# Kernel optimization log

Measured on AMD Instinct MI355X. Metric: run time of the kernel, lower is better.

## Reference

```python
import jax, jax.numpy as jnp
import numpy as np

T, B, I, H = 512, 256, 256, 512  # seq_len, batch, input_size, hidden_size


def setup_inputs() -> dict:
    key = jax.random.key(0)
    ks = jax.random.split(key, 7)
    sc = 1.0 / np.sqrt(H)  # PyTorch nn.RNN init scale ~ U(-1/sqrt(H), 1/sqrt(H)); use scaled normal
    return {
        "x": jax.random.normal(ks[0], (T, B, I), dtype=jnp.float32),
        "w_ih": jax.random.normal(ks[1], (H, I), dtype=jnp.float32) * sc,
        "w_hh": jax.random.normal(ks[2], (H, H), dtype=jnp.float32) * sc,
        "b_ih": jax.random.normal(ks[3], (H,), dtype=jnp.float32) * sc,
        "b_hh": jax.random.normal(ks[4], (H,), dtype=jnp.float32) * sc,
        "w_fc": jax.random.normal(ks[5], (I, H), dtype=jnp.float32) * sc,
        "b_fc": jax.random.normal(ks[6], (I,), dtype=jnp.float32) * sc,
    }


def reference(x, w_ih, w_hh, b_ih, b_hh, w_fc, b_fc):
    # Single-layer tanh RNN (h0 = 0): h_t = tanh(x_t W_ih^T + b_ih + h_{t-1} W_hh^T + b_hh)
    # Hoist the input projection out of the recurrence (one big GEMM).
    xp = jnp.einsum('tbi,hi->tbh', x, w_ih) + b_ih + b_hh  # [T,B,H]
    h0 = jnp.zeros((x.shape[1], w_hh.shape[0]), dtype=x.dtype)

    def step(h, xt):
        h_new = jnp.tanh(xt + h @ w_hh.T)
        return h_new, h_new

    _, hs = jax.lax.scan(step, h0, xp)  # hs: [T,B,H]
    # Output head: Linear(hidden_size -> input_size)
    return jnp.einsum('tbh,oh->tbo', hs, w_fc) + b_fc  # [T,B,I]
```

## Files before the change

### kernel.cpp

```cpp
#include <hip/hip_runtime.h>
#include <hip/hip_bf16.h>

#define T_ 512
#define B_ 256
#define I_ 256
#define H_ 512

#define NG 16
#define NS 4

#define RING_WPG (H_ * 8)
#define RING_BYTES (2ull * NG * RING_WPG * 8)

typedef _Float16 f16x8 __attribute__((ext_vector_type(8)));
typedef float f32x4 __attribute__((ext_vector_type(4)));

__device__ __forceinline__ float tanh_fast(float v) {
  float e = __expf(2.0f * v);
  return 1.0f - 2.0f / (e + 1.0f);
}

__device__ __forceinline__ f16x8 cvt8(const float4 a, const float4 b) {
  f16x8 f;
  f[0] = (_Float16)a.x; f[1] = (_Float16)a.y; f[2] = (_Float16)a.z; f[3] = (_Float16)a.w;
  f[4] = (_Float16)b.x; f[5] = (_Float16)b.y; f[6] = (_Float16)b.z; f[7] = (_Float16)b.w;
  return f;
}

__device__ __forceinline__ unsigned long long pack2h(_Float16 a, _Float16 b, unsigned tag) {
  unsigned ua = __builtin_bit_cast(unsigned short, a);
  unsigned ub = __builtin_bit_cast(unsigned short, b);
  return (unsigned long long)(ua | (ub << 16)) | ((unsigned long long)tag << 32);
}

__global__ __launch_bounds__(256, 1) void rnn_recurrence(
    const float* __restrict__ x,
    const float* __restrict__ w_ih,
    const float* __restrict__ w_hh,
    const float* __restrict__ b_ih,
    const float* __restrict__ b_hh,
    unsigned long long* __restrict__ ring,
    _Float16* __restrict__ hs)
{
  const int tid  = threadIdx.x;
  const int lane = tid & 63;
  const int w    = tid >> 6;
  const int bid  = blockIdx.x;
  const int g    = bid & 15;
  const int s    = bid >> 4;
  const int r0   = g * 16;
  const int c0   = s * 128;
  const int lrow = lane & 15;
  const int quad = lane >> 4;
  const int kq   = quad * 8;

  __shared__ _Float16 hbuf[16][512 + 8];
  __shared__ _Float16 xbuf[16][256 + 8];

  f16x8 whh0[16], whh1[16];
  f16x8 wih0[8], wih1[8];
  const int n0c = c0 + (2 * w + 0) * 16 + lrow;
  const int n1c = c0 + (2 * w + 1) * 16 + lrow;
  const float bias0 = b_ih[n0c] + b_hh[n0c];
  const float bias1 = b_ih[n1c] + b_hh[n1c];
  #pragma unroll
  for (int kt = 0; kt < 16; ++kt) {
    const int k = kt * 32 + kq;
    whh0[kt] = cvt8(*(const float4*)(w_hh + (size_t)n0c * H_ + k),
                    *(const float4*)(w_hh + (size_t)n0c * H_ + k + 4));
    whh1[kt] = cvt8(*(const float4*)(w_hh + (size_t)n1c * H_ + k),
                    *(const float4*)(w_hh + (size_t)n1c * H_ + k + 4));
  }
  #pragma unroll
  for (int kt = 0; kt < 8; ++kt) {
    const int k = kt * 32 + kq;
    wih0[kt] = cvt8(*(const float4*)(w_ih + (size_t)n0c * I_ + k),
                    *(const float4*)(w_ih + (size_t)n0c * I_ + k + 4));
    wih1[kt] = cvt8(*(const float4*)(w_ih + (size_t)n1c * I_ + k),
                    *(const float4*)(w_ih + (size_t)n1c * I_ + k + 4));
  }

  int colf[12], prow[12];
  int roff[12];
  #pragma unroll
  for (int j = 0; j < 12; ++j) {
    const int wdx = tid + j * 256;
    const int rs  = wdx >> 10;
    const int sl  = rs + (rs >= s ? 1 : 0);
    const int c   = (wdx >> 3) & 127;
    const int p   = wdx & 7;
    colf[j] = sl * 128 + c;
    prow[j] = p * 2;
    roff[j] = colf[j] * 8 + p;
  }

  {
    const int row = tid >> 4, ch = tid & 15;
    f16x8 z = {0, 0, 0, 0, 0, 0, 0, 0};
    *(f16x8*)(&hbuf[row][c0 + ch * 8]) = z;
  }

  for (int t = 0; t < T_; ++t) {
    {
      const float* src = x + ((size_t)t * B_ + r0) * I_;
      #pragma unroll
      for (int c = tid; c < 512; c += 256) {
        const int row = c >> 5;
        const int col = (c & 31) * 8;
        *(f16x8*)(&xbuf[row][col]) =
            cvt8(*(const float4*)(src + (size_t)row * I_ + col),
                 *(const float4*)(src + (size_t)row * I_ + col + 4));
      }
    }
    {
      const unsigned long long* rg =
          ring + ((size_t)((t & 1) ? NG : 0) + g) * RING_WPG;
      unsigned long long v[12];
      #pragma unroll
      for (int j = 0; j < 12; ++j)
        v[j] = __hip_atomic_load(&rg[roff[j]], __ATOMIC_RELAXED,
                                 __HIP_MEMORY_SCOPE_AGENT);
      bool again = true;
      while (again) {
        again = false;
        #pragma unroll
        for (int j = 0; j < 12; ++j) {
          if ((unsigned)(v[j] >> 32) != (unsigned)t) {
            v[j] = __hip_atomic_load(&rg[roff[j]], __ATOMIC_RELAXED,
                                     __HIP_MEMORY_SCOPE_AGENT);
            again = true;
          }
        }
      }
      #pragma unroll
      for (int j = 0; j < 12; ++j) {
        const unsigned lo = (unsigned)v[j];
        hbuf[prow[j] + 0][colf[j]] =
            __builtin_bit_cast(_Float16, (unsigned short)(lo & 0xffff));
        hbuf[prow[j] + 1][colf[j]] =
            __builtin_bit_cast(_Float16, (unsigned short)(lo >> 16));
      }
    }
    __syncthreads();

    if (t > 0) {
      const int row = tid >> 4, ch = tid & 15;
      *(uint4*)(hs + ((size_t)(t - 1) * B_ + r0 + row) * H_ + c0 + ch * 8) =
          *(const uint4*)(&hbuf[row][c0 + ch * 8]);
    }

    f32x4 a0a = {0.f,0.f,0.f,0.f}, a0b = {0.f,0.f,0.f,0.f};
    f32x4 a1a = {0.f,0.f,0.f,0.f}, a1b = {0.f,0.f,0.f,0.f};
    #pragma unroll
    for (int kt = 0; kt < 8; ++kt) {
      const f16x8 a = *(const f16x8*)(&hbuf[lrow][kt * 32 + kq]);
      a0a = __builtin_amdgcn_mfma_f32_16x16x32_f16(a, whh0[kt], a0a, 0, 0, 0);
      a1a = __builtin_amdgcn_mfma_f32_16x16x32_f16(a, whh1[kt], a1a, 0, 0, 0);
    }
    #pragma unroll
    for (int kt = 8; kt < 16; ++kt) {
      const f16x8 a = *(const f16x8*)(&hbuf[lrow][kt * 32 + kq]);
      a0b = __builtin_amdgcn_mfma_f32_16x16x32_f16(a, whh0[kt], a0b, 0, 0, 0);
      a1b = __builtin_amdgcn_mfma_f32_16x16x32_f16(a, whh1[kt], a1b, 0, 0, 0);
    }
    #pragma unroll
    for (int kt = 0; kt < 4; ++kt) {
      const f16x8 a = *(const f16x8*)(&xbuf[lrow][kt * 32 + kq]);
      a0a = __builtin_amdgcn_mfma_f32_16x16x32_f16(a, wih0[kt], a0a, 0, 0, 0);
      a1a = __builtin_amdgcn_mfma_f32_16x16x32_f16(a, wih1[kt], a1a, 0, 0, 0);
    }
    #pragma unroll
    for (int kt = 4; kt < 8; ++kt) {
      const f16x8 a = *(const f16x8*)(&xbuf[lrow][kt * 32 + kq]);
      a0b = __builtin_amdgcn_mfma_f32_16x16x32_f16(a, wih0[kt], a0b, 0, 0, 0);
      a1b = __builtin_amdgcn_mfma_f32_16x16x32_f16(a, wih1[kt], a1b, 0, 0, 0);
    }
    const f32x4 acc0 = a0a + a0b;
    const f32x4 acc1 = a1a + a1b;

    __syncthreads();

    _Float16 e0[4], e1[4];
    #pragma unroll
    for (int r = 0; r < 4; ++r) {
      e0[r] = (_Float16)tanh_fast(acc0[r] + bias0);
      e1[r] = (_Float16)tanh_fast(acc1[r] + bias1);
      hbuf[quad * 4 + r][n0c] = e0[r];
      hbuf[quad * 4 + r][n1c] = e1[r];
    }
    {
      unsigned long long* rn =
          ring + ((size_t)(((t + 1) & 1) ? NG : 0) + g) * RING_WPG;
      const unsigned tag = (unsigned)(t + 1);
      __hip_atomic_store(&rn[n0c * 8 + quad * 2 + 0], pack2h(e0[0], e0[1], tag),
                         __ATOMIC_RELAXED, __HIP_MEMORY_SCOPE_AGENT);
      __hip_atomic_store(&rn[n0c * 8 + quad * 2 + 1], pack2h(e0[2], e0[3], tag),
                         __ATOMIC_RELAXED, __HIP_MEMORY_SCOPE_AGENT);
      __hip_atomic_store(&rn[n1c * 8 + quad * 2 + 0], pack2h(e1[0], e1[1], tag),
                         __ATOMIC_RELAXED, __HIP_MEMORY_SCOPE_AGENT);
      __hip_atomic_store(&rn[n1c * 8 + quad * 2 + 1], pack2h(e1[2], e1[3], tag),
                         __ATOMIC_RELAXED, __HIP_MEMORY_SCOPE_AGENT);
    }
  }

  __syncthreads();
  {
    const int row = tid >> 4, ch = tid & 15;
    *(uint4*)(hs + ((size_t)(T_ - 1) * B_ + r0 + row) * H_ + c0 + ch * 8) =
        *(const uint4*)(&hbuf[row][c0 + ch * 8]);
  }
}

__global__ __launch_bounds__(256) void fc_head(
    const _Float16* __restrict__ hs,
    const float* __restrict__ w_fc,
    const float* __restrict__ b_fc,
    float* __restrict__ out)
{
  const int tid  = threadIdx.x;
  const int lane = tid & 63;
  const int w    = tid >> 6;
  const int wm   = w & 1;
  const int wn   = w >> 1;
  const int m0   = blockIdx.x * 64;
  const int n0   = blockIdx.y * 64;
  const int lrow = lane & 15;
  const int quad = lane >> 4;
  const int kq   = quad * 8;

  __shared__ _Float16 As[64][32 + 8];
  __shared__ _Float16 Bs[64][32 + 8];

  f32x4 acc00 = {0.f,0.f,0.f,0.f}, acc01 = {0.f,0.f,0.f,0.f};
  f32x4 acc10 = {0.f,0.f,0.f,0.f}, acc11 = {0.f,0.f,0.f,0.f};

  const int srow = tid >> 2;
  const int skc  = (tid & 3) * 8;

  for (int k0 = 0; k0 < H_; k0 += 32) {
    *(uint4*)(&As[srow][skc]) =
        *(const uint4*)(hs + (size_t)(m0 + srow) * H_ + k0 + skc);
    *(f16x8*)(&Bs[srow][skc]) =
        cvt8(*(const float4*)(w_fc + (size_t)(n0 + srow) * H_ + k0 + skc),
             *(const float4*)(w_fc + (size_t)(n0 + srow) * H_ + k0 + skc + 4));
    __syncthreads();

    const f16x8 a0 = *(const f16x8*)(&As[wm * 32 + lrow][kq]);
    const f16x8 a1 = *(const f16x8*)(&As[wm * 32 + 16 + lrow][kq]);
    const f16x8 b0 = *(const f16x8*)(&Bs[wn * 32 + lrow][kq]);
    const f16x8 b1 = *(const f16x8*)(&Bs[wn * 32 + 16 + lrow][kq]);
    acc00 = __builtin_amdgcn_mfma_f32_16x16x32_f16(a0, b0, acc00, 0, 0, 0);
    acc01 = __builtin_amdgcn_mfma_f32_16x16x32_f16(a0, b1, acc01, 0, 0, 0);
    acc10 = __builtin_amdgcn_mfma_f32_16x16x32_f16(a1, b0, acc10, 0, 0, 0);
    acc11 = __builtin_amdgcn_mfma_f32_16x16x32_f16(a1, b1, acc11, 0, 0, 0);
    __syncthreads();
  }

  #pragma unroll
  for (int ni = 0; ni < 2; ++ni) {
    const int col = n0 + wn * 32 + ni * 16 + lrow;
    const float bf = b_fc[col];
    #pragma unroll
    for (int mi = 0; mi < 2; ++mi) {
      const f32x4 a = (mi == 0) ? (ni == 0 ? acc00 : acc01)
                                : (ni == 0 ? acc10 : acc11);
      #pragma unroll
      for (int r = 0; r < 4; ++r) {
        const int rowm = m0 + wm * 32 + mi * 16 + quad * 4 + r;
        out[(size_t)rowm * I_ + col] = a[r] + bf;
      }
    }
  }
}

extern "C" void kernel_launch(void* const* d_in, const int* in_sizes, int n_in,
                              void* d_out, int out_size, void* d_ws, size_t ws_size,
                              hipStream_t stream) {
  const float* x    = (const float*)d_in[0];
  const float* w_ih = (const float*)d_in[1];
  const float* w_hh = (const float*)d_in[2];
  const float* b_ih = (const float*)d_in[3];
  const float* b_hh = (const float*)d_in[4];
  const float* w_fc = (const float*)d_in[5];
  const float* b_fc = (const float*)d_in[6];
  float* out = (float*)d_out;

  unsigned long long* ring = (unsigned long long*)d_ws;
  _Float16* hs = (_Float16*)((char*)d_ws + RING_BYTES);

  hipMemsetAsync(d_ws, 0, (size_t)NG * RING_WPG * 8, stream);

  rnn_recurrence<<<64, 256, 0, stream>>>(x, w_ih, w_hh, b_ih, b_hh, ring, hs);
  fc_head<<<dim3(2048, 4), 256, 0, stream>>>(hs, w_fc, b_fc, out);
}
```

Measured before the change: 1.999 ms.

## Split recurrence across two blocks per batch group and overlap own-half MFMA with ring wait

Each batch group of 16 rows now uses two 512-thread blocks, each owning 256 hidden columns, instead of four 256-thread blocks. Each block exchanges only one remote half through the ring rather than three remote quarters. The input projection and the hidden matmul over the block's own half run before it polls the ring, so the cross-block wait overlaps with compute. The x tile for the next step is prefetched into a double buffer, the hs store is moved earlier, and s_sleep backoff is added to the spin loop. Fewer, larger blocks cut communication fan-in but leave more work per CU on the serial critical path.

```diff
diff --git a/kernel.cpp b/kernel.cpp
--- a/kernel.cpp
+++ b/kernel.cpp
@@ -7,10 +7,10 @@
 #define H_ 512
 
 #define NG 16
-#define NS 4
-
-#define RING_WPG (H_ * 8)
-#define RING_BYTES (2ull * NG * RING_WPG * 8)
+#define NSL 2
+
+#define RWORDS 2048
+#define RING_BYTES (2ull * NG * NSL * RWORDS * 8)
 
 typedef _Float16 f16x8 __attribute__((ext_vector_type(8)));
 typedef float f32x4 __attribute__((ext_vector_type(4)));
@@ -33,7 +33,7 @@
   return (unsigned long long)(ua | (ub << 16)) | ((unsigned long long)tag << 32);
 }
 
-__global__ __launch_bounds__(256, 1) void rnn_recurrence(
+__global__ __launch_bounds__(512, 1) void rnn_recurrence(
     const float* __restrict__ x,
     const float* __restrict__ w_ih,
     const float* __restrict__ w_hh,
@@ -46,16 +46,19 @@
   const int lane = tid & 63;
   const int w    = tid >> 6;
   const int bid  = blockIdx.x;
-  const int g    = bid & 15;
-  const int s    = bid >> 4;
+  const int g    = bid >> 1;
+  const int s    = bid & 1;
   const int r0   = g * 16;
-  const int c0   = s * 128;
+  const int c0   = s * 256;
+  const int rc0  = (s ^ 1) * 256;
   const int lrow = lane & 15;
   const int quad = lane >> 4;
   const int kq   = quad * 8;
+  const int ktO  = s * 8;
+  const int ktR  = (s ^ 1) * 8;
 
   __shared__ _Float16 hbuf[16][512 + 8];
-  __shared__ _Float16 xbuf[16][256 + 8];
+  __shared__ _Float16 xbuf[2][16][256 + 8];
 
   f16x8 whh0[16], whh1[16];
   f16x8 wih0[8], wih1[8];
@@ -80,100 +83,110 @@
                     *(const float4*)(w_ih + (size_t)n1c * I_ + k + 4));
   }
 
-  int colf[12], prow[12];
-  int roff[12];
-  #pragma unroll
-  for (int j = 0; j < 12; ++j) {
-    const int wdx = tid + j * 256;
-    const int rs  = wdx >> 10;
-    const int sl  = rs + (rs >= s ? 1 : 0);
-    const int c   = (wdx >> 3) & 127;
-    const int p   = wdx & 7;
-    colf[j] = sl * 128 + c;
-    prow[j] = p * 2;
-    roff[j] = colf[j] * 8 + p;
-  }
-
   {
-    const int row = tid >> 4, ch = tid & 15;
+    const int row = tid >> 5, ch = tid & 31;
     f16x8 z = {0, 0, 0, 0, 0, 0, 0, 0};
     *(f16x8*)(&hbuf[row][c0 + ch * 8]) = z;
+    const float* src = x + (size_t)(r0 + row) * I_;
+    *(f16x8*)(&xbuf[0][row][ch * 8]) =
+        cvt8(*(const float4*)(src + ch * 8), *(const float4*)(src + ch * 8 + 4));
   }
 
   for (int t = 0; t < T_; ++t) {
-    {
-      const float* src = x + ((size_t)t * B_ + r0) * I_;
-      #pragma unroll
-      for (int c = tid; c < 512; c += 256) {
-        const int row = c >> 5;
-        const int col = (c & 31) * 8;
-        *(f16x8*)(&xbuf[row][col]) =
-            cvt8(*(const float4*)(src + (size_t)row * I_ + col),
-                 *(const float4*)(src + (size_t)row * I_ + col + 4));
-      }
-    }
+    const int xb = t & 1;
+    __syncthreads();
+
+    if (t + 1 < T_) {
+      const int row = tid >> 5, ch = tid & 31;
+      const float* src = x + ((size_t)(t + 1) * B_ + r0 + row) * I_;
+      *(f16x8*)(&xbuf[xb ^ 1][row][ch * 8]) =
+          cvt8(*(const float4*)(src + ch * 8), *(const float4*)(src + ch * 8 + 4));
+    }
+    if (t > 0) {
+      const int row = tid >> 5, ch = tid & 31;
+      *(uint4*)(hs + ((size_t)(t - 1) * B_ + r0 + row) * H_ + c0 + ch * 8) =
+          *(const uint4*)(&hbuf[row][c0 + ch * 8]);
+    }
+
+    f32x4 a0a = {0.f,0.f,0.f,0.f}, a0b = {0.f,0.f,0.f,0.f};
+    f32x4 a1a = {0.f,0.f,0.f,0.f}, a1b = {0.f,0.f,0.f,0.f};
+    #pragma unroll
+    for (int kt = 0; kt < 4; ++kt) {
+      const f16x8 a = *(const f16x8*)(&xbuf[xb][lrow][kt * 32 + kq]);
+      a0a = __builtin_amdgcn_mfma_f32_16x16x32_f16(a, wih0[kt], a0a, 0, 0, 0);
+      a1a = __builtin_amdgcn_mfma_f32_16x16x32_f16(a, wih1[kt], a1a, 0, 0, 0);
+    }
+    #pragma unroll
+    for (int kt = 4; kt < 8; ++kt) {
+      const f16x8 a = *(const f16x8*)(&xbuf[xb][lrow][kt * 32 + kq]);
+      a0b = __builtin_amdgcn_mfma_f32_16x16x32_f16(a, wih0[kt], a0b, 0, 0, 0);
+      a1b = __builtin_amdgcn_mfma_f32_16x16x32_f16(a, wih1[kt], a1b, 0, 0, 0);
+    }
+    #pragma unroll
+    for (int kk = 0; kk < 4; ++kk) {
+      const int kt = ktO + kk;
+      const f16x8 a = *(const f16x8*)(&hbuf[lrow][kt * 32 + kq]);
+      a0a = __builtin_amdgcn_mfma_f32_16x16x32_f16(a, whh0[kt], a0a, 0, 0, 0);
+      a1a = __builtin_amdgcn_mfma_f32_16x16x32_f16(a, whh1[kt], a1a, 0, 0, 0);
+    }
+    #pragma unroll
+    for (int kk = 4; kk < 8; ++kk) {
+      const int kt = ktO + kk;
+      const f16x8 a = *(const f16x8*)(&hbuf[lrow][kt * 32 + kq]);
+      a0b = __builtin_amdgcn_mfma_f32_16x16x32_f16(a, whh0[kt], a0b, 0, 0, 0);
+      a1b = __builtin_amdgcn_mfma_f32_16x16x32_f16(a, whh1[kt], a1b, 0, 0, 0);
+    }
+
     {
       const unsigned long long* rg =
-          ring + ((size_t)((t & 1) ? NG : 0) + g) * RING_WPG;
-      unsigned long long v[12];
+          ring + (((size_t)(t & 1) * NG + g) * NSL + (s ^ 1)) * RWORDS;
+      unsigned long long v[4];
       #pragma unroll
-      for (int j = 0; j < 12; ++j)
-        v[j] = __hip_atomic_load(&rg[roff[j]], __ATOMIC_RELAXED,
+      for (int j = 0; j < 4; ++j)
+        v[j] = __hip_atomic_load(&rg[tid * 4 + j], __ATOMIC_RELAXED,
                                  __HIP_MEMORY_SCOPE_AGENT);
+      int spins = 0;
       bool again = true;
       while (again) {
         again = false;
         #pragma unroll
-        for (int j = 0; j < 12; ++j) {
-          if ((unsigned)(v[j] >> 32) != (unsigned)t) {
-            v[j] = __hip_atomic_load(&rg[roff[j]], __ATOMIC_RELAXED,
-                                     __HIP_MEMORY_SCOPE_AGENT);
-            again = true;
-          }
+        for (int j = 0; j < 4; ++j)
+          if ((unsigned)(v[j] >> 32) != (unsigned)t) again = true;
+        if (again) {
+          if (spins++) __builtin_amdgcn_s_sleep(1);
+          #pragma unroll
+          for (int j = 0; j < 4; ++j)
+            if ((unsigned)(v[j] >> 32) != (unsigned)t)
+              v[j] = __hip_atomic_load(&rg[tid * 4 + j], __ATOMIC_RELAXED,
+                                       __HIP_MEMORY_SCOPE_AGENT);
         }
       }
       #pragma unroll
-      for (int j = 0; j < 12; ++j) {
+      for (int j = 0; j < 4; ++j) {
+        const int wdx = tid * 4 + j;
+        const int col = rc0 + (wdx >> 3);
+        const int p   = wdx & 7;
+        const int r   = 4 * (p >> 1) + 2 * (p & 1);
         const unsigned lo = (unsigned)v[j];
-        hbuf[prow[j] + 0][colf[j]] =
-            __builtin_bit_cast(_Float16, (unsigned short)(lo & 0xffff));
-        hbuf[prow[j] + 1][colf[j]] =
-            __builtin_bit_cast(_Float16, (unsigned short)(lo >> 16));
+        hbuf[r + 0][col] = __builtin_bit_cast(_Float16, (unsigned short)(lo & 0xffff));
+        hbuf[r + 1][col] = __builtin_bit_cast(_Float16, (unsigned short)(lo >> 16));
       }
     }
     __syncthreads();
 
-    if (t > 0) {
-      const int row = tid >> 4, ch = tid & 15;
-      *(uint4*)(hs + ((size_t)(t - 1) * B_ + r0 + row) * H_ + c0 + ch * 8) =
-          *(const uint4*)(&hbuf[row][c0 + ch * 8]);
-    }
-
-    f32x4 a0a = {0.f,0.f,0.f,0.f}, a0b = {0.f,0.f,0.f,0.f};
-    f32x4 a1a = {0.f,0.f,0.f,0.f}, a1b = {0.f,0.f,0.f,0.f};
-    #pragma unroll
-    for (int kt = 0; kt < 8; ++kt) {
+    #pragma unroll
+    for (int kk = 0; kk < 4; ++kk) {
+      const int kt = ktR + kk;
       const f16x8 a = *(const f16x8*)(&hbuf[lrow][kt * 32 + kq]);
       a0a = __builtin_amdgcn_mfma_f32_16x16x32_f16(a, whh0[kt], a0a, 0, 0, 0);
       a1a = __builtin_amdgcn_mfma_f32_16x16x32_f16(a, whh1[kt], a1a, 0, 0, 0);
     }
     #pragma unroll
-    for (int kt = 8; kt < 16; ++kt) {
+    for (int kk = 4; kk < 8; ++kk) {
+      const int kt = ktR + kk;
       const f16x8 a = *(const f16x8*)(&hbuf[lrow][kt * 32 + kq]);
       a0b = __builtin_amdgcn_mfma_f32_16x16x32_f16(a, whh0[kt], a0b, 0, 0, 0);
       a1b = __builtin_amdgcn_mfma_f32_16x16x32_f16(a, whh1[kt], a1b, 0, 0, 0);
-    }
-    #pragma unroll
-    for (int kt = 0; kt < 4; ++kt) {
-      const f16x8 a = *(const f16x8*)(&xbuf[lrow][kt * 32 + kq]);
-      a0a = __builtin_amdgcn_mfma_f32_16x16x32_f16(a, wih0[kt], a0a, 0, 0, 0);
-      a1a = __builtin_amdgcn_mfma_f32_16x16x32_f16(a, wih1[kt], a1a, 0, 0, 0);
-    }
-    #pragma unroll
-    for (int kt = 4; kt < 8; ++kt) {
-      const f16x8 a = *(const f16x8*)(&xbuf[lrow][kt * 32 + kq]);
-      a0b = __builtin_amdgcn_mfma_f32_16x16x32_f16(a, wih0[kt], a0b, 0, 0, 0);
-      a1b = __builtin_amdgcn_mfma_f32_16x16x32_f16(a, wih1[kt], a1b, 0, 0, 0);
     }
     const f32x4 acc0 = a0a + a0b;
     const f32x4 acc1 = a1a + a1b;
@@ -190,22 +203,24 @@
     }
     {
       unsigned long long* rn =
-          ring + ((size_t)(((t + 1) & 1) ? NG : 0) + g) * RING_WPG;
+          ring + (((size_t)((t + 1) & 1) * NG + g) * NSL + s) * RWORDS;
       const unsigned tag = (unsigned)(t + 1);
-      __hip_atomic_store(&rn[n0c * 8 + quad * 2 + 0], pack2h(e0[0], e0[1], tag),
+      const int o0 = (n0c - c0) * 8 + quad * 2;
+      const int o1 = (n1c - c0) * 8 + quad * 2;
+      __hip_atomic_store(&rn[o0 + 0], pack2h(e0[0], e0[1], tag),
                          __ATOMIC_RELAXED, __HIP_MEMORY_SCOPE_AGENT);
-      __hip_atomic_store(&rn[n0c * 8 + quad * 2 + 1], pack2h(e0[2], e0[3], tag),
+      __hip_atomic_store(&rn[o0 + 1], pack2h(e0[2], e0[3], tag),
                          __ATOMIC_RELAXED, __HIP_MEMORY_SCOPE_AGENT);
-      __hip_atomic_store(&rn[n1c * 8 + quad * 2 + 0], pack2h(e1[0], e1[1], tag),
+      __hip_atomic_store(&rn[o1 + 0], pack2h(e1[0], e1[1], tag),
                          __ATOMIC_RELAXED, __HIP_MEMORY_SCOPE_AGENT);
-      __hip_atomic_store(&rn[n1c * 8 + quad * 2 + 1], pack2h(e1[2], e1[3], tag),
+      __hip_atomic_store(&rn[o1 + 1], pack2h(e1[2], e1[3], tag),
                          __ATOMIC_RELAXED, __HIP_MEMORY_SCOPE_AGENT);
     }
   }
 
   __syncthreads();
   {
-    const int row = tid >> 4, ch = tid & 15;
+    const int row = tid >> 5, ch = tid & 31;
     *(uint4*)(hs + ((size_t)(T_ - 1) * B_ + r0 + row) * H_ + c0 + ch * 8) =
         *(const uint4*)(&hbuf[row][c0 + ch * 8]);
   }
@@ -288,8 +303,8 @@
   unsigned long long* ring = (unsigned long long*)d_ws;
   _Float16* hs = (_Float16*)((char*)d_ws + RING_BYTES);
 
-  hipMemsetAsync(d_ws, 0, (size_t)NG * RING_WPG * 8, stream);
-
-  rnn_recurrence<<<64, 256, 0, stream>>>(x, w_ih, w_hh, b_ih, b_hh, ring, hs);
+  hipMemsetAsync(d_ws, 0, (size_t)NG * NSL * RWORDS * 8, stream);
+
+  rnn_recurrence<<<32, 512, 0, stream>>>(x, w_ih, w_hh, b_ih, b_hh, ring, hs);
   fc_head<<<dim3(2048, 4), 256, 0, stream>>>(hs, w_fc, b_fc, out);
 }
```

Result: slower. 4.791 ms (+139.6%).
